# Optimization experiments

Measured on AMD Instinct MI355X. Metric: run time of the kernel, lower is better.

## Reference

```python
import jax, jax.numpy as jnp
import numpy as np

VOCAB = 200000
D = 128
B, P, R = 256, 64, 32
EPS = 1e-8


def _cos(a, b):
    # torch CosineSimilarity(dim=-1, eps=1e-8): clamp norms
    na = jnp.maximum(jnp.linalg.norm(a, axis=-1), EPS)
    nb = jnp.maximum(jnp.linalg.norm(b, axis=-1), EPS)
    return jnp.sum(a * b, axis=-1) / (na * nb)


def setup_inputs() -> dict:
    key = jax.random.key(0)
    ks = jax.random.split(key, 16)
    s = 1.0 / np.sqrt(D)
    inp = {
        "support_path": jax.random.randint(ks[0], (B, P, 3), 0, VOCAB - 1),
        "support_pair": jax.random.randint(ks[1], (B, 2), 0, VOCAB - 1),
        "support_relation_set": jax.random.randint(ks[2], (B, R), 0, VOCAB - 1),
        "emb": jax.random.normal(ks[3], (VOCAB, D), jnp.float32),
        "w_d_w": jax.random.uniform(ks[4], (D, D), jnp.float32, -s, s),
        "w_d_b": jax.random.uniform(ks[5], (D,), jnp.float32, -s, s),
        "w_e_w": jax.random.uniform(ks[6], (D, D), jnp.float32, -s, s),
        "w_e_b": jax.random.uniform(ks[7], (D,), jnp.float32, -s, s),
        "w_p_w": jax.random.uniform(ks[8], (D, D), jnp.float32, -s, s),
        "w_p_b": jax.random.uniform(ks[9], (D,), jnp.float32, -s, s),
        "e_u_w": jax.random.uniform(ks[10], (1, D), jnp.float32, -s, s),
        "e_u_b": jax.random.uniform(ks[11], (1,), jnp.float32, -s, s),
        "gru_w_ih": jax.random.uniform(ks[12], (3 * D, D), jnp.float32, -s, s),
        "gru_w_hh": jax.random.uniform(ks[13], (3 * D, D), jnp.float32, -s, s),
        "gru_b_ih": jax.random.uniform(ks[14], (3 * D,), jnp.float32, -s, s),
        "gru_b_hh": jax.random.uniform(ks[15], (3 * D,), jnp.float32, -s, s),
    }
    return inp


def _gru_cell(x, h, w_ih, w_hh, b_ih, b_hh):
    gi = x @ w_ih.T + b_ih
    gh = h @ w_hh.T + b_hh
    i_r, i_z, i_n = jnp.split(gi, 3, axis=-1)
    h_r, h_z, h_n = jnp.split(gh, 3, axis=-1)
    r = jax.nn.sigmoid(i_r + h_r)
    z = jax.nn.sigmoid(i_z + h_z)
    n = jnp.tanh(i_n + r * h_n)
    return (1.0 - z) * n + z * h


def reference(support_path, support_pair, support_relation_set, emb,
              w_d_w, w_d_b, w_e_w, w_e_b, w_p_w, w_p_b,
              e_u_w, e_u_b, gru_w_ih, gru_w_hh, gru_b_ih, gru_b_hh):
    head_emb = emb[support_pair[:, 0]]          # [B, D]
    tail_emb = emb[support_pair[:, 1]]          # [B, D]
    hts = _cos(head_emb, tail_emb)              # [B], head-tail sim per group

    rel_emb = emb[support_path]                 # [B, P, 3, D] per-step relation embeddings
    relset_emb = emb[support_relation_set]      # [B, R, D]

    # attention denominator over the group's relation set
    exp_set = jnp.exp(relset_emb @ e_u_w.T + e_u_b)        # [B, R, 1]
    sum_exp = jnp.sum(exp_set, axis=1, keepdims=True)      # [B, 1, 1]

    # entity_1/entity_2 are read from the path tensor in the original code
    e1 = rel_emb[:, :, 0, :]                                # [B, P, D]
    e2 = rel_emb[:, :, 1, :]
    h_b = head_emb[:, None, :]                              # [B, 1, D]
    t_b = tail_emb[:, None, :]
    sim_e1 = 0.5 * (_cos(h_b, e1) + _cos(t_b, e1))          # [B, P]
    sim_e2 = 0.5 * (_cos(h_b, e2) + _cos(t_b, e2))
    hts_b = hts[:, None]
    sim_rel = jnp.stack([
        0.5 * (hts_b + sim_e1),
        0.5 * (sim_e1 + sim_e2),
        0.5 * (hts_b + sim_e2),
    ], axis=-1)                                             # [B, P, 3]
    sim_dist = (1.0 - sim_rel) / 2.0                        # [B, P, 3]

    # attention score per path step
    e_score = jnp.exp(rel_emb @ e_u_w.T + e_u_b) / sum_exp[:, :, None, :]  # [B, P, 3, 1]

    d_in = rel_emb * sim_dist[..., None]
    e_in = rel_emb * e_score
    d_out = d_in @ w_d_w.T + w_d_b
    e_out = e_in @ w_e_w.T + w_e_b
    cost = 0.001 * jax.nn.relu(d_out + e_out)               # [B, P, 3, D]

    # GRU over 3 path steps, zero initial hidden
    rel_in = (rel_emb - cost) @ w_p_w.T + w_p_b             # [B, P, 3, D]
    x_steps = jnp.moveaxis(rel_in.reshape(B * P, 3, D), 1, 0)  # [3, B*P, D]

    def step(h, x):
        h2 = _gru_cell(x, h, gru_w_ih, gru_w_hh, gru_b_ih, gru_b_hh)
        return h2, None

    h0 = jnp.zeros((B * P, D), rel_in.dtype)
    h_final, _ = jax.lax.scan(step, h0, x_steps)
    return h_final.reshape(B, P, D)
```

## Files before the change

kernel.cpp:

```cpp
#include <hip/hip_runtime.h>
#include <cmath>

#define D_ 128
#define B_ 256
#define P_ 64
#define R_ 32
#define NROW (B_*P_*3)
#define NBP  (B_*P_)
#define GROWS 192
#define EPS_ 1e-8f

typedef unsigned short u16;
typedef unsigned int   u32;
using bf16x8 = __attribute__((ext_vector_type(8))) __bf16;
using f32x4  = __attribute__((ext_vector_type(4))) float;

__device__ __forceinline__ float sigm_f(float x){ return 1.0f/(1.0f + __expf(-x)); }
__device__ __forceinline__ float tanh_f(float x){
    float e = __expf(2.0f*x);
    return 1.0f - 2.0f/(e + 1.0f);
}

__device__ __forceinline__ u16 f2b(float f){
    u32 u = __builtin_bit_cast(u32, f);
    u += 0x7fffu + ((u >> 16) & 1u);
    return (u16)(u >> 16);
}
__device__ __forceinline__ float b2f(u16 s){
    return __builtin_bit_cast(float, ((u32)s) << 16);
}
__device__ __forceinline__ bf16x8 pack8(float a0,float a1,float a2,float a3,
                                        float a4,float a5,float a6,float a7){
    uint4 r;
    r.x = (u32)f2b(a0) | ((u32)f2b(a1) << 16);
    r.y = (u32)f2b(a2) | ((u32)f2b(a3) << 16);
    r.z = (u32)f2b(a4) | ((u32)f2b(a5) << 16);
    r.w = (u32)f2b(a6) | ((u32)f2b(a7) << 16);
    return __builtin_bit_cast(bf16x8, r);
}
__device__ __forceinline__ bf16x8 ldg8(const u16* p){
    return __builtin_bit_cast(bf16x8, *(const uint4*)p);
}
__device__ __forceinline__ bf16x8 ldA(const u16* Xs, int row, int gk){
    return __builtin_bit_cast(bf16x8,
        *(const uint4*)(&Xs[row*128 + ((gk ^ (row & 7)) << 3)]));
}
__device__ __forceinline__ int swz_slot(int row, int col){
    return row*128 + (((col >> 3) ^ (row & 7)) << 3) + (col & 7);
}

__global__ __launch_bounds__(1024) void k_wcvt(
    const float* __restrict__ wd, const float* __restrict__ we,
    const float* __restrict__ wp, const float* __restrict__ wih,
    const float* __restrict__ whh,
    u16* __restrict__ wdb, u16* __restrict__ web, u16* __restrict__ wpb,
    u16* __restrict__ wib, u16* __restrict__ whb)
{
    int i = blockIdx.x*1024 + threadIdx.x;
    int e = i*8;
    const float* src; u16* dst; int off;
    if      (e < 16384) { src = wd;  dst = wdb; off = e; }
    else if (e < 32768) { src = we;  dst = web; off = e - 16384; }
    else if (e < 49152) { src = wp;  dst = wpb; off = e - 32768; }
    else if (e < 98304) { src = wih; dst = wib; off = e - 49152; }
    else                { src = whh; dst = whb; off = e - 98304; }
    float4 a = *(const float4*)(src + off);
    float4 b = *(const float4*)(src + off + 4);
    uint4 r;
    r.x = (u32)f2b(a.x) | ((u32)f2b(a.y) << 16);
    r.y = (u32)f2b(a.z) | ((u32)f2b(a.w) << 16);
    r.z = (u32)f2b(b.x) | ((u32)f2b(b.y) << 16);
    r.w = (u32)f2b(b.z) | ((u32)f2b(b.w) << 16);
    *(uint4*)(dst + off) = r;
}

__global__ __launch_bounds__(512,2) void k_mega(
    const int* __restrict__ pair, const int* __restrict__ relset,
    const int* __restrict__ path,
    const float* __restrict__ emb, const float* __restrict__ eu,
    const float* __restrict__ eub,
    const u16* __restrict__ wdb, const float* __restrict__ bd,
    const u16* __restrict__ web, const float* __restrict__ be,
    const u16* __restrict__ wpb, const float* __restrict__ bpv_,
    const u16* __restrict__ wib, const u16* __restrict__ whb,
    const float* __restrict__ bih, const float* __restrict__ bhh,
    float* __restrict__ out)
{
    __shared__ u16   Xs[GROWS*128];
    __shared__ u16   Hs[64*128];
    __shared__ int   pS[GROWS];
    __shared__ float pdh[GROWS], pdt[GROWS], pdu[GROWS], pnn[GROWS];
    __shared__ float sdS[GROWS], seS[GROWS];
    __shared__ float s_hts, s_hi, s_ti;
    __shared__ float s_part[8];

    const int b    = blockIdx.x;
    const int tid  = threadIdx.x;
    const int wave = tid >> 6, lane = tid & 63;
    const int lrow = lane & 15, lk8 = lane >> 4;
    const int col  = wave*16 + lrow;
    const float eb = eub[0];

    if (tid < GROWS) pS[tid] = path[b*GROWS + tid];
    bf16x8 fD[4], fE[4], fP[4];
    #pragma unroll
    for (int ks = 0; ks < 4; ++ks) {
        const int gk = ks*4 + lk8;
        fD[ks] = ldg8(wdb + col*128 + gk*8);
        fE[ks] = ldg8(web + col*128 + gk*8);
        fP[ks] = ldg8(wpb + col*128 + gk*8);
    }
    const int ph = pair[2*b], ptl = pair[2*b+1];
    __syncthreads();

    {
        #pragma unroll
        for (int i = 0; i < 6; ++i) {
            int gid = i*512 + tid;
            int r = gid >> 4, g = gid & 15;
            const float* sp = emb + (size_t)pS[r]*128 + g*8;
            float4 f0 = *(const float4*)sp;
            float4 f1 = *(const float4*)(sp + 4);
            bf16x8 v = pack8(f0.x,f0.y,f0.z,f0.w, f1.x,f1.y,f1.z,f1.w);
            *(uint4*)(&Xs[r*128 + ((g ^ (r & 7)) << 3)]) = __builtin_bit_cast(uint4, v);
        }
        if (wave == 0) {
            float2 hv2 = *(const float2*)(emb + (size_t)ph*128 + 2*lane);
            float2 tv2 = *(const float2*)(emb + (size_t)ptl*128 + 2*lane);
            float dht = hv2.x*tv2.x + hv2.y*tv2.y;
            float dhh = hv2.x*hv2.x + hv2.y*hv2.y;
            float dtt = tv2.x*tv2.x + tv2.y*tv2.y;
            #pragma unroll
            for (int o = 32; o > 0; o >>= 1) {
                dht += __shfl_xor(dht, o);
                dhh += __shfl_xor(dhh, o);
                dtt += __shfl_xor(dtt, o);
            }
            if (lane == 0) {
                float hn = 1.f / fmaxf(sqrtf(dhh), EPS_);
                float tn = 1.f / fmaxf(sqrtf(dtt), EPS_);
                s_hts = dht*hn*tn;
                s_hi  = hn;
                s_ti  = tn;
            }
        }
        float2 uv2 = *(const float2*)(eu + 2*lane);
        float accs = 0.f;
        #pragma unroll
        for (int k = 0; k < 4; ++k) {
            const int ri = relset[b*R_ + wave*4 + k];
            float2 ev = *(const float2*)(emb + (size_t)ri*128 + 2*lane);
            float du = ev.x*uv2.x + ev.y*uv2.y;
            #pragma unroll
            for (int o = 32; o > 0; o >>= 1) du += __shfl_xor(du, o);
            accs += __expf(du + eb);
        }
        if (lane == 0) s_part[wave] = accs;
    }
    __syncthreads();

    {
        const int sub = lane >> 4, l16 = lane & 15;
        const float* hpq = emb + (size_t)ph*128  + l16*8;
        const float* tpq = emb + (size_t)ptl*128 + l16*8;
        const float* upq = eu + l16*8;
        float hq[8], tq[8], uq[8];
        {
            float4 a0 = *(const float4*)hpq, a1 = *(const float4*)(hpq+4);
            float4 b0 = *(const float4*)tpq, b1 = *(const float4*)(tpq+4);
            float4 c0 = *(const float4*)upq, c1 = *(const float4*)(upq+4);
            hq[0]=a0.x;hq[1]=a0.y;hq[2]=a0.z;hq[3]=a0.w;hq[4]=a1.x;hq[5]=a1.y;hq[6]=a1.z;hq[7]=a1.w;
            tq[0]=b0.x;tq[1]=b0.y;tq[2]=b0.z;tq[3]=b0.w;tq[4]=b1.x;tq[5]=b1.y;tq[6]=b1.z;tq[7]=b1.w;
            uq[0]=c0.x;uq[1]=c0.y;uq[2]=c0.z;uq[3]=c0.w;uq[4]=c1.x;uq[5]=c1.y;uq[6]=c1.z;uq[7]=c1.w;
        }
        #pragma unroll
        for (int i = 0; i < 6; ++i) {
            const int r = wave*24 + i*4 + sub;
            uint4 gv = *(const uint4*)(&Xs[r*128 + ((l16 ^ (r & 7)) << 3)]);
            float v[8];
            v[0]=b2f((u16)(gv.x&0xffff)); v[1]=b2f((u16)(gv.x>>16));
            v[2]=b2f((u16)(gv.y&0xffff)); v[3]=b2f((u16)(gv.y>>16));
            v[4]=b2f((u16)(gv.z&0xffff)); v[5]=b2f((u16)(gv.z>>16));
            v[6]=b2f((u16)(gv.w&0xffff)); v[7]=b2f((u16)(gv.w>>16));
            float dh=0.f, dt=0.f, du=0.f, nn=0.f;
            #pragma unroll
            for (int j = 0; j < 8; ++j) {
                dh = fmaf(v[j], hq[j], dh);
                dt = fmaf(v[j], tq[j], dt);
                du = fmaf(v[j], uq[j], du);
                nn = fmaf(v[j], v[j], nn);
            }
            #pragma unroll
            for (int o = 8; o > 0; o >>= 1) {
                dh += __shfl_xor(dh, o);
                dt += __shfl_xor(dt, o);
                du += __shfl_xor(du, o);
                nn += __shfl_xor(nn, o);
            }
            if (l16 == 0) { pdh[r]=dh; pdt[r]=dt; pdu[r]=du; pnn[r]=nn; }
        }
    }
    __syncthreads();

    if (tid < 64) {
        float is = 0.f;
        #pragma unroll
        for (int w = 0; w < 8; ++w) is += s_part[w];
        is = 1.f/is;
        const float hi = s_hi, ti = s_ti, ht = s_hts;
        const int r1 = 3*tid, r2 = r1+1, r3 = r1+2;
        float n1i = 1.f / fmaxf(sqrtf(pnn[r1]), EPS_);
        float n2i = 1.f / fmaxf(sqrtf(pnn[r2]), EPS_);
        float se1 = 0.5f*(pdh[r1]*hi + pdt[r1]*ti)*n1i;
        float se2 = 0.5f*(pdh[r2]*hi + pdt[r2]*ti)*n2i;
        sdS[r1] = (1.f - 0.5f*(ht  + se1))*0.5f;
        sdS[r2] = (1.f - 0.5f*(se1 + se2))*0.5f;
        sdS[r3] = (1.f - 0.5f*(ht  + se2))*0.5f;
        seS[r1] = expf(pdu[r1] + eb)*is;
        seS[r2] = expf(pdu[r2] + eb)*is;
        seS[r3] = expf(pdu[r3] + eb)*is;
    }
    __syncthreads();

    {
        f32x4 aD[12], aE[12];
        #pragma unroll
        for (int m = 0; m < 12; ++m) { aD[m] = (f32x4){0,0,0,0}; aE[m] = (f32x4){0,0,0,0}; }
        #pragma unroll
        for (int ks = 0; ks < 4; ++ks) {
            const int gk = ks*4 + lk8;
            #pragma unroll
            for (int mt = 0; mt < 12; ++mt) {
                bf16x8 a = ldA(Xs, mt*16 + lrow, gk);
                aD[mt] = __builtin_amdgcn_mfma_f32_16x16x32_bf16(a, fD[ks], aD[mt], 0,0,0);
                aE[mt] = __builtin_amdgcn_mfma_f32_16x16x32_bf16(a, fE[ks], aE[mt], 0,0,0);
            }
        }
        __syncthreads();
        const float bde = bd[col] + be[col];
        #pragma unroll
        for (int mt = 0; mt < 12; ++mt) {
            #pragma unroll
            for (int rr = 0; rr < 4; ++rr) {
                const int row = mt*16 + lk8*4 + rr;
                const int sl  = swz_slot(row, col);
                float relv = b2f(Xs[sl]);
                float c = sdS[row]*aD[mt][rr] + seS[row]*aE[mt][rr] + bde;
                Xs[sl] = f2b(relv - 1e-3f*fmaxf(c, 0.f));
            }
        }
    }
    __syncthreads();

    {
        f32x4 aP[12];
        #pragma unroll
        for (int m = 0; m < 12; ++m) aP[m] = (f32x4){0,0,0,0};
        #pragma unroll
        for (int ks = 0; ks < 4; ++ks) {
            const int gk = ks*4 + lk8;
            #pragma unroll
            for (int mt = 0; mt < 12; ++mt) {
                bf16x8 a = ldA(Xs, mt*16 + lrow, gk);
                aP[mt] = __builtin_amdgcn_mfma_f32_16x16x32_bf16(a, fP[ks], aP[mt], 0,0,0);
            }
        }
        __syncthreads();
        const float bpv = bpv_[col];
        #pragma unroll
        for (int mt = 0; mt < 12; ++mt) {
            #pragma unroll
            for (int rr = 0; rr < 4; ++rr) {
                const int row = mt*16 + lk8*4 + rr;
                Xs[swz_slot(row, col)] = f2b(aP[mt][rr] + bpv);
            }
        }
    }
    __syncthreads();

    bf16x8 wR[4], wZ[4], wI[4], vR[4], vZ[4], vH[4];
    #pragma unroll
    for (int ks = 0; ks < 4; ++ks) {
        const int gk = ks*4 + lk8;
        wR[ks] = ldg8(wib +           col*128 + gk*8);
        wZ[ks] = ldg8(wib + 16384   + col*128 + gk*8);
        wI[ks] = ldg8(wib + 2*16384 + col*128 + gk*8);
        vR[ks] = ldg8(whb +           col*128 + gk*8);
        vZ[ks] = ldg8(whb + 16384   + col*128 + gk*8);
        vH[ks] = ldg8(whb + 2*16384 + col*128 + gk*8);
    }
    const float brv = bih[col]       + bhh[col];
    const float bzv = bih[128 + col] + bhh[128 + col];
    const float biN = bih[256 + col];
    const float bhN = bhh[256 + col];

    float hreg[4][4];
    f32x4 aR[4], aZ[4], aI[4], aH[4];

    #pragma unroll
    for (int m = 0; m < 4; ++m) { aR[m]=(f32x4){0,0,0,0}; aZ[m]=(f32x4){0,0,0,0}; aI[m]=(f32x4){0,0,0,0}; }
    #pragma unroll
    for (int ks = 0; ks < 4; ++ks) {
        const int gk = ks*4 + lk8;
        #pragma unroll
        for (int mt = 0; mt < 4; ++mt) {
            bf16x8 ax = ldA(Xs, 3*(mt*16 + lrow) + 0, gk);
            aR[mt] = __builtin_amdgcn_mfma_f32_16x16x32_bf16(ax, wR[ks], aR[mt], 0,0,0);
            aZ[mt] = __builtin_amdgcn_mfma_f32_16x16x32_bf16(ax, wZ[ks], aZ[mt], 0,0,0);
            aI[mt] = __builtin_amdgcn_mfma_f32_16x16x32_bf16(ax, wI[ks], aI[mt], 0,0,0);
        }
    }
    #pragma unroll
    for (int mt = 0; mt < 4; ++mt)
        #pragma unroll
        for (int rr = 0; rr < 4; ++rr) {
            const int row = mt*16 + lk8*4 + rr;
            float rv = sigm_f(aR[mt][rr] + brv);
            float zv = sigm_f(aZ[mt][rr] + bzv);
            float nn = tanh_f(aI[mt][rr] + biN + rv*bhN);
            float h2 = (1.f - zv)*nn;
            hreg[mt][rr] = h2;
            Hs[swz_slot(row, col)] = f2b(h2);
        }
    __syncthreads();

    #pragma unroll
    for (int m = 0; m < 4; ++m) { aR[m]=(f32x4){0,0,0,0}; aZ[m]=(f32x4){0,0,0,0}; aI[m]=(f32x4){0,0,0,0}; aH[m]=(f32x4){0,0,0,0}; }
    #pragma unroll
    for (int ks = 0; ks < 4; ++ks) {
        const int gk = ks*4 + lk8;
        #pragma unroll
        for (int mt = 0; mt < 4; ++mt) {
            bf16x8 ax = ldA(Xs, 3*(mt*16 + lrow) + 1, gk);
            bf16x8 ah = ldA(Hs, mt*16 + lrow, gk);
            aR[mt] = __builtin_amdgcn_mfma_f32_16x16x32_bf16(ax, wR[ks], aR[mt], 0,0,0);
            aZ[mt] = __builtin_amdgcn_mfma_f32_16x16x32_bf16(ax, wZ[ks], aZ[mt], 0,0,0);
            aI[mt] = __builtin_amdgcn_mfma_f32_16x16x32_bf16(ax, wI[ks], aI[mt], 0,0,0);
            aR[mt] = __builtin_amdgcn_mfma_f32_16x16x32_bf16(ah, vR[ks], aR[mt], 0,0,0);
            aZ[mt] = __builtin_amdgcn_mfma_f32_16x16x32_bf16(ah, vZ[ks], aZ[mt], 0,0,0);
            aH[mt] = __builtin_amdgcn_mfma_f32_16x16x32_bf16(ah, vH[ks], aH[mt], 0,0,0);
        }
    }
    __syncthreads();
    #pragma unroll
    for (int mt = 0; mt < 4; ++mt)
        #pragma unroll
        for (int rr = 0; rr < 4; ++rr) {
            const int row = mt*16 + lk8*4 + rr;
            float rv = sigm_f(aR[mt][rr] + brv);
            float zv = sigm_f(aZ[mt][rr] + bzv);
            float hn = aH[mt][rr] + bhN;
            float nn = tanh_f(aI[mt][rr] + biN + rv*hn);
            float h2 = (1.f - zv)*nn + zv*hreg[mt][rr];
            hreg[mt][rr] = h2;
            Hs[swz_slot(row, col)] = f2b(h2);
        }
    __syncthreads();

    #pragma unroll
    for (int m = 0; m < 4; ++m) { aR[m]=(f32x4){0,0,0,0}; aZ[m]=(f32x4){0,0,0,0}; aI[m]=(f32x4){0,0,0,0}; aH[m]=(f32x4){0,0,0,0}; }
    #pragma unroll
    for (int ks = 0; ks < 4; ++ks) {
        const int gk = ks*4 + lk8;
        #pragma unroll
        for (int mt = 0; mt < 4; ++mt) {
            bf16x8 ax = ldA(Xs, 3*(mt*16 + lrow) + 2, gk);
            bf16x8 ah = ldA(Hs, mt*16 + lrow, gk);
            aR[mt] = __builtin_amdgcn_mfma_f32_16x16x32_bf16(ax, wR[ks], aR[mt], 0,0,0);
            aZ[mt] = __builtin_amdgcn_mfma_f32_16x16x32_bf16(ax, wZ[ks], aZ[mt], 0,0,0);
            aI[mt] = __builtin_amdgcn_mfma_f32_16x16x32_bf16(ax, wI[ks], aI[mt], 0,0,0);
            aR[mt] = __builtin_amdgcn_mfma_f32_16x16x32_bf16(ah, vR[ks], aR[mt], 0,0,0);
            aZ[mt] = __builtin_amdgcn_mfma_f32_16x16x32_bf16(ah, vZ[ks], aZ[mt], 0,0,0);
            aH[mt] = __builtin_amdgcn_mfma_f32_16x16x32_bf16(ah, vH[ks], aH[mt], 0,0,0);
        }
    }
    const int bp0 = b*64;
    #pragma unroll
    for (int mt = 0; mt < 4; ++mt)
        #pragma unroll
        for (int rr = 0; rr < 4; ++rr) {
            const int row = mt*16 + lk8*4 + rr;
            float rv = sigm_f(aR[mt][rr] + brv);
            float zv = sigm_f(aZ[mt][rr] + bzv);
            float hn = aH[mt][rr] + bhN;
            float nn = tanh_f(aI[mt][rr] + biN + rv*hn);
            float h2 = (1.f - zv)*nn + zv*hreg[mt][rr];
            out[(size_t)(bp0 + row)*128 + col] = h2;
        }
}

extern "C" void kernel_launch(void* const* d_in, const int* in_sizes, int n_in,
                              void* d_out, int out_size, void* d_ws, size_t ws_size,
                              hipStream_t stream)
{
    const int*   path   = (const int*)d_in[0];
    const int*   pair   = (const int*)d_in[1];
    const int*   relset = (const int*)d_in[2];
    const float* emb    = (const float*)d_in[3];
    const float* wd     = (const float*)d_in[4];
    const float* bd     = (const float*)d_in[5];
    const float* we     = (const float*)d_in[6];
    const float* be     = (const float*)d_in[7];
    const float* wp     = (const float*)d_in[8];
    const float* bp     = (const float*)d_in[9];
    const float* eu     = (const float*)d_in[10];
    const float* eub    = (const float*)d_in[11];
    const float* wih    = (const float*)d_in[12];
    const float* whh    = (const float*)d_in[13];
    const float* bih    = (const float*)d_in[14];
    const float* bhh    = (const float*)d_in[15];
    float* out = (float*)d_out;
    float* ws  = (float*)d_ws;

    u16* wdb = (u16*)ws;
    u16* web = wdb + 16384;
    u16* wpb = web + 16384;
    u16* wib = wpb + 16384;
    u16* whb = wib + 49152;

    k_wcvt<<<18, 1024, 0, stream>>>(wd, we, wp, wih, whh, wdb, web, wpb, wib, whb);
    k_mega<<<B_, 512, 0, stream>>>(pair, relset, path, emb, eu, eub,
                                   wdb, bd, web, be, wpb, bp,
                                   wib, whb, bih, bhh, out);
}
```

Measured before the change: 48.12 us.

## Split each batch across two blocks and fuse weight conversion into main kernel

Each batch element is now handled by two blocks of 32 paths each, doubling the grid to 512 blocks and halving shared memory and accumulator registers per block so occupancy can rise to four blocks per CU. The separate fp32-to-bf16 weight conversion kernel is removed; weights are loaded as fp32 and packed to bf16 inside the main kernel right before each GEMM, which drops one launch. Hidden-weight fragments are reloaded per GRU step to cut register pressure. In exchange every block redoes the weight conversion and the per-batch head/tail/relation-set reductions, adding redundant global loads and ALU work.

```diff
diff --git a/kernel.cpp b/kernel.cpp
--- a/kernel.cpp
+++ b/kernel.cpp
@@ -5,9 +5,7 @@
 #define B_ 256
 #define P_ 64
 #define R_ 32
-#define NROW (B_*P_*3)
-#define NBP  (B_*P_)
-#define GROWS 192
+#define HROWS 96
 #define EPS_ 1e-8f
 
 typedef unsigned short u16;
@@ -38,8 +36,10 @@
     r.w = (u32)f2b(a6) | ((u32)f2b(a7) << 16);
     return __builtin_bit_cast(bf16x8, r);
 }
-__device__ __forceinline__ bf16x8 ldg8(const u16* p){
-    return __builtin_bit_cast(bf16x8, *(const uint4*)p);
+__device__ __forceinline__ bf16x8 ldw8(const float* p){
+    float4 a = *(const float4*)p;
+    float4 b = *(const float4*)(p + 4);
+    return pack8(a.x,a.y,a.z,a.w, b.x,b.y,b.z,b.w);
 }
 __device__ __forceinline__ bf16x8 ldA(const u16* Xs, int row, int gk){
     return __builtin_bit_cast(bf16x8,
@@ -49,73 +49,42 @@
     return row*128 + (((col >> 3) ^ (row & 7)) << 3) + (col & 7);
 }
 
-__global__ __launch_bounds__(1024) void k_wcvt(
-    const float* __restrict__ wd, const float* __restrict__ we,
-    const float* __restrict__ wp, const float* __restrict__ wih,
-    const float* __restrict__ whh,
-    u16* __restrict__ wdb, u16* __restrict__ web, u16* __restrict__ wpb,
-    u16* __restrict__ wib, u16* __restrict__ whb)
-{
-    int i = blockIdx.x*1024 + threadIdx.x;
-    int e = i*8;
-    const float* src; u16* dst; int off;
-    if      (e < 16384) { src = wd;  dst = wdb; off = e; }
-    else if (e < 32768) { src = we;  dst = web; off = e - 16384; }
-    else if (e < 49152) { src = wp;  dst = wpb; off = e - 32768; }
-    else if (e < 98304) { src = wih; dst = wib; off = e - 49152; }
-    else                { src = whh; dst = whb; off = e - 98304; }
-    float4 a = *(const float4*)(src + off);
-    float4 b = *(const float4*)(src + off + 4);
-    uint4 r;
-    r.x = (u32)f2b(a.x) | ((u32)f2b(a.y) << 16);
-    r.y = (u32)f2b(a.z) | ((u32)f2b(a.w) << 16);
-    r.z = (u32)f2b(b.x) | ((u32)f2b(b.y) << 16);
-    r.w = (u32)f2b(b.z) | ((u32)f2b(b.w) << 16);
-    *(uint4*)(dst + off) = r;
-}
-
-__global__ __launch_bounds__(512,2) void k_mega(
+__global__ __launch_bounds__(512,4) void k_mega(
     const int* __restrict__ pair, const int* __restrict__ relset,
     const int* __restrict__ path,
     const float* __restrict__ emb, const float* __restrict__ eu,
     const float* __restrict__ eub,
-    const u16* __restrict__ wdb, const float* __restrict__ bd,
-    const u16* __restrict__ web, const float* __restrict__ be,
-    const u16* __restrict__ wpb, const float* __restrict__ bpv_,
-    const u16* __restrict__ wib, const u16* __restrict__ whb,
+    const float* __restrict__ wd, const float* __restrict__ bd,
+    const float* __restrict__ we, const float* __restrict__ be,
+    const float* __restrict__ wp, const float* __restrict__ bpv_,
+    const float* __restrict__ wih, const float* __restrict__ whh,
     const float* __restrict__ bih, const float* __restrict__ bhh,
     float* __restrict__ out)
 {
-    __shared__ u16   Xs[GROWS*128];
-    __shared__ u16   Hs[64*128];
-    __shared__ int   pS[GROWS];
-    __shared__ float pdh[GROWS], pdt[GROWS], pdu[GROWS], pnn[GROWS];
-    __shared__ float sdS[GROWS], seS[GROWS];
+    __shared__ u16   Xs[HROWS*128];
+    __shared__ u16   Hs[32*128];
+    __shared__ int   pS[HROWS];
+    __shared__ float pdh[HROWS], pdt[HROWS], pdu[HROWS], pnn[HROWS];
+    __shared__ float sdS[HROWS], seS[HROWS];
     __shared__ float s_hts, s_hi, s_ti;
     __shared__ float s_part[8];
 
-    const int b    = blockIdx.x;
+    const int blk  = blockIdx.x;
+    const int b    = blk >> 1;
+    const int hb   = blk & 1;
     const int tid  = threadIdx.x;
     const int wave = tid >> 6, lane = tid & 63;
     const int lrow = lane & 15, lk8 = lane >> 4;
     const int col  = wave*16 + lrow;
     const float eb = eub[0];
 
-    if (tid < GROWS) pS[tid] = path[b*GROWS + tid];
-    bf16x8 fD[4], fE[4], fP[4];
-    #pragma unroll
-    for (int ks = 0; ks < 4; ++ks) {
-        const int gk = ks*4 + lk8;
-        fD[ks] = ldg8(wdb + col*128 + gk*8);
-        fE[ks] = ldg8(web + col*128 + gk*8);
-        fP[ks] = ldg8(wpb + col*128 + gk*8);
-    }
+    if (tid < HROWS) pS[tid] = path[b*192 + hb*HROWS + tid];
     const int ph = pair[2*b], ptl = pair[2*b+1];
     __syncthreads();
 
     {
         #pragma unroll
-        for (int i = 0; i < 6; ++i) {
+        for (int i = 0; i < 3; ++i) {
             int gid = i*512 + tid;
             int r = gid >> 4, g = gid & 15;
             const float* sp = emb + (size_t)pS[r]*128 + g*8;
@@ -160,7 +129,8 @@
     __syncthreads();
 
     {
-        const int sub = lane >> 4, l16 = lane & 15;
+        const int grp = tid >> 4;
+        const int l16 = tid & 15;
         const float* hpq = emb + (size_t)ph*128  + l16*8;
         const float* tpq = emb + (size_t)ptl*128 + l16*8;
         const float* upq = eu + l16*8;
@@ -174,8 +144,8 @@
             uq[0]=c0.x;uq[1]=c0.y;uq[2]=c0.z;uq[3]=c0.w;uq[4]=c1.x;uq[5]=c1.y;uq[6]=c1.z;uq[7]=c1.w;
         }
         #pragma unroll
-        for (int i = 0; i < 6; ++i) {
-            const int r = wave*24 + i*4 + sub;
+        for (int i = 0; i < 3; ++i) {
+            const int r = i*32 + grp;
             uint4 gv = *(const uint4*)(&Xs[r*128 + ((l16 ^ (r & 7)) << 3)]);
             float v[8];
             v[0]=b2f((u16)(gv.x&0xffff)); v[1]=b2f((u16)(gv.x>>16));
@@ -202,7 +172,7 @@
     }
     __syncthreads();
 
-    if (tid < 64) {
+    if (tid < 32) {
         float is = 0.f;
         #pragma unroll
         for (int w = 0; w < 8; ++w) is += s_part[w];
@@ -223,14 +193,21 @@
     __syncthreads();
 
     {
-        f32x4 aD[12], aE[12];
-        #pragma unroll
-        for (int m = 0; m < 12; ++m) { aD[m] = (f32x4){0,0,0,0}; aE[m] = (f32x4){0,0,0,0}; }
-        #pragma unroll
-        for (int ks = 0; ks < 4; ++ks) {
-            const int gk = ks*4 + lk8;
-            #pragma unroll
-            for (int mt = 0; mt < 12; ++mt) {
+        bf16x8 fD[4], fE[4];
+        #pragma unroll
+        for (int ks = 0; ks < 4; ++ks) {
+            const int gk = ks*4 + lk8;
+            fD[ks] = ldw8(wd + col*128 + gk*8);
+            fE[ks] = ldw8(we + col*128 + gk*8);
+        }
+        f32x4 aD[6], aE[6];
+        #pragma unroll
+        for (int m = 0; m < 6; ++m) { aD[m] = (f32x4){0,0,0,0}; aE[m] = (f32x4){0,0,0,0}; }
+        #pragma unroll
+        for (int ks = 0; ks < 4; ++ks) {
+            const int gk = ks*4 + lk8;
+            #pragma unroll
+            for (int mt = 0; mt < 6; ++mt) {
                 bf16x8 a = ldA(Xs, mt*16 + lrow, gk);
                 aD[mt] = __builtin_amdgcn_mfma_f32_16x16x32_bf16(a, fD[ks], aD[mt], 0,0,0);
                 aE[mt] = __builtin_amdgcn_mfma_f32_16x16x32_bf16(a, fE[ks], aE[mt], 0,0,0);
@@ -239,7 +216,7 @@
         __syncthreads();
         const float bde = bd[col] + be[col];
         #pragma unroll
-        for (int mt = 0; mt < 12; ++mt) {
+        for (int mt = 0; mt < 6; ++mt) {
             #pragma unroll
             for (int rr = 0; rr < 4; ++rr) {
                 const int row = mt*16 + lk8*4 + rr;
@@ -253,14 +230,20 @@
     __syncthreads();
 
     {
-        f32x4 aP[12];
-        #pragma unroll
-        for (int m = 0; m < 12; ++m) aP[m] = (f32x4){0,0,0,0};
-        #pragma unroll
-        for (int ks = 0; ks < 4; ++ks) {
-            const int gk = ks*4 + lk8;
-            #pragma unroll
-            for (int mt = 0; mt < 12; ++mt) {
+        bf16x8 fP[4];
+        #pragma unroll
+        for (int ks = 0; ks < 4; ++ks) {
+            const int gk = ks*4 + lk8;
+            fP[ks] = ldw8(wp + col*128 + gk*8);
+        }
+        f32x4 aP[6];
+        #pragma unroll
+        for (int m = 0; m < 6; ++m) aP[m] = (f32x4){0,0,0,0};
+        #pragma unroll
+        for (int ks = 0; ks < 4; ++ks) {
+            const int gk = ks*4 + lk8;
+            #pragma unroll
+            for (int mt = 0; mt < 6; ++mt) {
                 bf16x8 a = ldA(Xs, mt*16 + lrow, gk);
                 aP[mt] = __builtin_amdgcn_mfma_f32_16x16x32_bf16(a, fP[ks], aP[mt], 0,0,0);
             }
@@ -268,7 +251,7 @@
         __syncthreads();
         const float bpv = bpv_[col];
         #pragma unroll
-        for (int mt = 0; mt < 12; ++mt) {
+        for (int mt = 0; mt < 6; ++mt) {
             #pragma unroll
             for (int rr = 0; rr < 4; ++rr) {
                 const int row = mt*16 + lk8*4 + rr;
@@ -278,32 +261,29 @@
     }
     __syncthreads();
 
-    bf16x8 wR[4], wZ[4], wI[4], vR[4], vZ[4], vH[4];
+    bf16x8 wR[4], wZ[4], wI[4];
     #pragma unroll
     for (int ks = 0; ks < 4; ++ks) {
         const int gk = ks*4 + lk8;
-        wR[ks] = ldg8(wib +           col*128 + gk*8);
-        wZ[ks] = ldg8(wib + 16384   + col*128 + gk*8);
-        wI[ks] = ldg8(wib + 2*16384 + col*128 + gk*8);
-        vR[ks] = ldg8(whb +           col*128 + gk*8);
-        vZ[ks] = ldg8(whb + 16384   + col*128 + gk*8);
-        vH[ks] = ldg8(whb + 2*16384 + col*128 + gk*8);
+        wR[ks] = ldw8(wih + (size_t)(      col)*128 + gk*8);
+        wZ[ks] = ldw8(wih + (size_t)(128 + col)*128 + gk*8);
+        wI[ks] = ldw8(wih + (size_t)(256 + col)*128 + gk*8);
     }
     const float brv = bih[col]       + bhh[col];
     const float bzv = bih[128 + col] + bhh[128 + col];
     const float biN = bih[256 + col];
     const float bhN = bhh[256 + col];
 
-    float hreg[4][4];
-    f32x4 aR[4], aZ[4], aI[4], aH[4];
-
-    #pragma unroll
-    for (int m = 0; m < 4; ++m) { aR[m]=(f32x4){0,0,0,0}; aZ[m]=(f32x4){0,0,0,0}; aI[m]=(f32x4){0,0,0,0}; }
+    float hreg[2][4];
+    f32x4 aR[2], aZ[2], aI[2], aH[2];
+
+    #pragma unroll
+    for (int m = 0; m < 2; ++m) { aR[m]=(f32x4){0,0,0,0}; aZ[m]=(f32x4){0,0,0,0}; aI[m]=(f32x4){0,0,0,0}; }
     #pragma unroll
     for (int ks = 0; ks < 4; ++ks) {
         const int gk = ks*4 + lk8;
         #pragma unroll
-        for (int mt = 0; mt < 4; ++mt) {
+        for (int mt = 0; mt < 2; ++mt) {
             bf16x8 ax = ldA(Xs, 3*(mt*16 + lrow) + 0, gk);
             aR[mt] = __builtin_amdgcn_mfma_f32_16x16x32_bf16(ax, wR[ks], aR[mt], 0,0,0);
             aZ[mt] = __builtin_amdgcn_mfma_f32_16x16x32_bf16(ax, wZ[ks], aZ[mt], 0,0,0);
@@ -311,7 +291,7 @@
         }
     }
     #pragma unroll
-    for (int mt = 0; mt < 4; ++mt)
+    for (int mt = 0; mt < 2; ++mt)
         #pragma unroll
         for (int rr = 0; rr < 4; ++rr) {
             const int row = mt*16 + lk8*4 + rr;
@@ -325,68 +305,59 @@
     __syncthreads();
 
     #pragma unroll
-    for (int m = 0; m < 4; ++m) { aR[m]=(f32x4){0,0,0,0}; aZ[m]=(f32x4){0,0,0,0}; aI[m]=(f32x4){0,0,0,0}; aH[m]=(f32x4){0,0,0,0}; }
-    #pragma unroll
-    for (int ks = 0; ks < 4; ++ks) {
-        const int gk = ks*4 + lk8;
-        #pragma unroll
-        for (int mt = 0; mt < 4; ++mt) {
-            bf16x8 ax = ldA(Xs, 3*(mt*16 + lrow) + 1, gk);
-            bf16x8 ah = ldA(Hs, mt*16 + lrow, gk);
-            aR[mt] = __builtin_amdgcn_mfma_f32_16x16x32_bf16(ax, wR[ks], aR[mt], 0,0,0);
-            aZ[mt] = __builtin_amdgcn_mfma_f32_16x16x32_bf16(ax, wZ[ks], aZ[mt], 0,0,0);
-            aI[mt] = __builtin_amdgcn_mfma_f32_16x16x32_bf16(ax, wI[ks], aI[mt], 0,0,0);
-            aR[mt] = __builtin_amdgcn_mfma_f32_16x16x32_bf16(ah, vR[ks], aR[mt], 0,0,0);
-            aZ[mt] = __builtin_amdgcn_mfma_f32_16x16x32_bf16(ah, vZ[ks], aZ[mt], 0,0,0);
-            aH[mt] = __builtin_amdgcn_mfma_f32_16x16x32_bf16(ah, vH[ks], aH[mt], 0,0,0);
-        }
-    }
-    __syncthreads();
-    #pragma unroll
-    for (int mt = 0; mt < 4; ++mt)
-        #pragma unroll
-        for (int rr = 0; rr < 4; ++rr) {
-            const int row = mt*16 + lk8*4 + rr;
-            float rv = sigm_f(aR[mt][rr] + brv);
-            float zv = sigm_f(aZ[mt][rr] + bzv);
-            float hn = aH[mt][rr] + bhN;
-            float nn = tanh_f(aI[mt][rr] + biN + rv*hn);
-            float h2 = (1.f - zv)*nn + zv*hreg[mt][rr];
-            hreg[mt][rr] = h2;
-            Hs[swz_slot(row, col)] = f2b(h2);
-        }
-    __syncthreads();
-
-    #pragma unroll
-    for (int m = 0; m < 4; ++m) { aR[m]=(f32x4){0,0,0,0}; aZ[m]=(f32x4){0,0,0,0}; aI[m]=(f32x4){0,0,0,0}; aH[m]=(f32x4){0,0,0,0}; }
-    #pragma unroll
-    for (int ks = 0; ks < 4; ++ks) {
-        const int gk = ks*4 + lk8;
-        #pragma unroll
-        for (int mt = 0; mt < 4; ++mt) {
-            bf16x8 ax = ldA(Xs, 3*(mt*16 + lrow) + 2, gk);
-            bf16x8 ah = ldA(Hs, mt*16 + lrow, gk);
-            aR[mt] = __builtin_amdgcn_mfma_f32_16x16x32_bf16(ax, wR[ks], aR[mt], 0,0,0);
-            aZ[mt] = __builtin_amdgcn_mfma_f32_16x16x32_bf16(ax, wZ[ks], aZ[mt], 0,0,0);
-            aI[mt] = __builtin_amdgcn_mfma_f32_16x16x32_bf16(ax, wI[ks], aI[mt], 0,0,0);
-            aR[mt] = __builtin_amdgcn_mfma_f32_16x16x32_bf16(ah, vR[ks], aR[mt], 0,0,0);
-            aZ[mt] = __builtin_amdgcn_mfma_f32_16x16x32_bf16(ah, vZ[ks], aZ[mt], 0,0,0);
-            aH[mt] = __builtin_amdgcn_mfma_f32_16x16x32_bf16(ah, vH[ks], aH[mt], 0,0,0);
-        }
-    }
-    const int bp0 = b*64;
-    #pragma unroll
-    for (int mt = 0; mt < 4; ++mt)
-        #pragma unroll
-        for (int rr = 0; rr < 4; ++rr) {
-            const int row = mt*16 + lk8*4 + rr;
-            float rv = sigm_f(aR[mt][rr] + brv);
-            float zv = sigm_f(aZ[mt][rr] + bzv);
-            float hn = aH[mt][rr] + bhN;
-            float nn = tanh_f(aI[mt][rr] + biN + rv*hn);
-            float h2 = (1.f - zv)*nn + zv*hreg[mt][rr];
-            out[(size_t)(bp0 + row)*128 + col] = h2;
-        }
+    for (int t = 1; t < 3; ++t) {
+        #pragma unroll
+        for (int m = 0; m < 2; ++m) { aR[m]=(f32x4){0,0,0,0}; aZ[m]=(f32x4){0,0,0,0}; aI[m]=(f32x4){0,0,0,0}; aH[m]=(f32x4){0,0,0,0}; }
+        #pragma unroll
+        for (int ks = 0; ks < 4; ++ks) {
+            const int gk = ks*4 + lk8;
+            bf16x8 vRk = ldw8(whh + (size_t)(      col)*128 + gk*8);
+            bf16x8 vZk = ldw8(whh + (size_t)(128 + col)*128 + gk*8);
+            bf16x8 vHk = ldw8(whh + (size_t)(256 + col)*128 + gk*8);
+            #pragma unroll
+            for (int mt = 0; mt < 2; ++mt) {
+                bf16x8 ax = ldA(Xs, 3*(mt*16 + lrow) + t, gk);
+                bf16x8 ah = ldA(Hs, mt*16 + lrow, gk);
+                aR[mt] = __builtin_amdgcn_mfma_f32_16x16x32_bf16(ax, wR[ks], aR[mt], 0,0,0);
+                aZ[mt] = __builtin_amdgcn_mfma_f32_16x16x32_bf16(ax, wZ[ks], aZ[mt], 0,0,0);
+                aI[mt] = __builtin_amdgcn_mfma_f32_16x16x32_bf16(ax, wI[ks], aI[mt], 0,0,0);
+                aR[mt] = __builtin_amdgcn_mfma_f32_16x16x32_bf16(ah, vRk, aR[mt], 0,0,0);
+                aZ[mt] = __builtin_amdgcn_mfma_f32_16x16x32_bf16(ah, vZk, aZ[mt], 0,0,0);
+                aH[mt] = __builtin_amdgcn_mfma_f32_16x16x32_bf16(ah, vHk, aH[mt], 0,0,0);
+            }
+        }
+        __syncthreads();
+        if (t < 2) {
+            #pragma unroll
+            for (int mt = 0; mt < 2; ++mt)
+                #pragma unroll
+                for (int rr = 0; rr < 4; ++rr) {
+                    const int row = mt*16 + lk8*4 + rr;
+                    float rv = sigm_f(aR[mt][rr] + brv);
+                    float zv = sigm_f(aZ[mt][rr] + bzv);
+                    float hn = aH[mt][rr] + bhN;
+                    float nn = tanh_f(aI[mt][rr] + biN + rv*hn);
+                    float h2 = (1.f - zv)*nn + zv*hreg[mt][rr];
+                    hreg[mt][rr] = h2;
+                    Hs[swz_slot(row, col)] = f2b(h2);
+                }
+            __syncthreads();
+        } else {
+            const int bp0 = b*64 + hb*32;
+            #pragma unroll
+            for (int mt = 0; mt < 2; ++mt)
+                #pragma unroll
+                for (int rr = 0; rr < 4; ++rr) {
+                    const int row = mt*16 + lk8*4 + rr;
+                    float rv = sigm_f(aR[mt][rr] + brv);
+                    float zv = sigm_f(aZ[mt][rr] + bzv);
+                    float hn = aH[mt][rr] + bhN;
+                    float nn = tanh_f(aI[mt][rr] + biN + rv*hn);
+                    float h2 = (1.f - zv)*nn + zv*hreg[mt][rr];
+                    out[(size_t)(bp0 + row)*128 + col] = h2;
+                }
+        }
+    }
 }
 
 extern "C" void kernel_launch(void* const* d_in, const int* in_sizes, int n_in,
@@ -410,16 +381,8 @@
     const float* bih    = (const float*)d_in[14];
     const float* bhh    = (const float*)d_in[15];
     float* out = (float*)d_out;
-    float* ws  = (float*)d_ws;
-
-    u16* wdb = (u16*)ws;
-    u16* web = wdb + 16384;
-    u16* wpb = web + 16384;
-    u16* wib = wpb + 16384;
-    u16* whb = wib + 49152;
-
-    k_wcvt<<<18, 1024, 0, stream>>>(wd, we, wp, wih, whh, wdb, web, wpb, wib, whb);
-    k_mega<<<B_, 512, 0, stream>>>(pair, relset, path, emb, eu, eub,
-                                   wdb, bd, web, be, wpb, bp,
-                                   wib, whb, bih, bhh, out);
-}
+
+    k_mega<<<2*B_, 512, 0, stream>>>(pair, relset, path, emb, eu, eub,
+                                     wd, bd, we, be, wp, bp,
+                                     wih, whh, bih, bhh, out);
+}
```

Result: slower. 80.85 us (+68.0%).

## Cut register pressure via per-tile GEMM loops, double LDS buffer, streamed GRU weights

Applied to the files above, without the earlier changes.

Restructures the D/E and P projection stages to process one 16-row tile at a time with small accumulators, writing the D/E result into a second LDS buffer (X2) so no barrier is needed between the MMA loads and the write-back. Weight fragments for the P projection and the GRU hidden-state weights are now loaded just before use rather than held in registers for the whole kernel, and the two GRU recurrence steps are folded into a loop. The intent is to lower VGPR pressure and avoid spills at 512 threads × 2 blocks, and to remove some barriers. In exchange, LDS use grows by 48KB per block, which may cut the number of resident blocks per CU, and the hidden-state weights are re-read from global/L2 on each step.

```diff
diff --git a/kernel.cpp b/kernel.cpp
--- a/kernel.cpp
+++ b/kernel.cpp
@@ -5,8 +5,6 @@
 #define B_ 256
 #define P_ 64
 #define R_ 32
-#define NROW (B_*P_*3)
-#define NBP  (B_*P_)
 #define GROWS 192
 #define EPS_ 1e-8f
 
@@ -87,6 +85,7 @@
     float* __restrict__ out)
 {
     __shared__ u16   Xs[GROWS*128];
+    __shared__ u16   X2[GROWS*128];
     __shared__ u16   Hs[64*128];
     __shared__ int   pS[GROWS];
     __shared__ float pdh[GROWS], pdt[GROWS], pdu[GROWS], pnn[GROWS];
@@ -102,13 +101,12 @@
     const float eb = eub[0];
 
     if (tid < GROWS) pS[tid] = path[b*GROWS + tid];
-    bf16x8 fD[4], fE[4], fP[4];
+    bf16x8 fD[4], fE[4];
     #pragma unroll
     for (int ks = 0; ks < 4; ++ks) {
         const int gk = ks*4 + lk8;
         fD[ks] = ldg8(wdb + col*128 + gk*8);
         fE[ks] = ldg8(web + col*128 + gk*8);
-        fP[ks] = ldg8(wpb + col*128 + gk*8);
     }
     const int ph = pair[2*b], ptl = pair[2*b+1];
     __syncthreads();
@@ -223,76 +221,65 @@
     __syncthreads();
 
     {
-        f32x4 aD[12], aE[12];
-        #pragma unroll
-        for (int m = 0; m < 12; ++m) { aD[m] = (f32x4){0,0,0,0}; aE[m] = (f32x4){0,0,0,0}; }
-        #pragma unroll
-        for (int ks = 0; ks < 4; ++ks) {
-            const int gk = ks*4 + lk8;
-            #pragma unroll
-            for (int mt = 0; mt < 12; ++mt) {
+        const float bde = bd[col] + be[col];
+        #pragma unroll 2
+        for (int mt = 0; mt < 12; ++mt) {
+            f32x4 aD = (f32x4){0,0,0,0}, aE = (f32x4){0,0,0,0};
+            #pragma unroll
+            for (int ks = 0; ks < 4; ++ks) {
+                const int gk = ks*4 + lk8;
                 bf16x8 a = ldA(Xs, mt*16 + lrow, gk);
-                aD[mt] = __builtin_amdgcn_mfma_f32_16x16x32_bf16(a, fD[ks], aD[mt], 0,0,0);
-                aE[mt] = __builtin_amdgcn_mfma_f32_16x16x32_bf16(a, fE[ks], aE[mt], 0,0,0);
-            }
-        }
-        __syncthreads();
-        const float bde = bd[col] + be[col];
-        #pragma unroll
-        for (int mt = 0; mt < 12; ++mt) {
+                aD = __builtin_amdgcn_mfma_f32_16x16x32_bf16(a, fD[ks], aD, 0,0,0);
+                aE = __builtin_amdgcn_mfma_f32_16x16x32_bf16(a, fE[ks], aE, 0,0,0);
+            }
             #pragma unroll
             for (int rr = 0; rr < 4; ++rr) {
                 const int row = mt*16 + lk8*4 + rr;
                 const int sl  = swz_slot(row, col);
                 float relv = b2f(Xs[sl]);
-                float c = sdS[row]*aD[mt][rr] + seS[row]*aE[mt][rr] + bde;
-                Xs[sl] = f2b(relv - 1e-3f*fmaxf(c, 0.f));
+                float c = sdS[row]*aD[rr] + seS[row]*aE[rr] + bde;
+                X2[sl] = f2b(relv - 1e-3f*fmaxf(c, 0.f));
             }
         }
     }
     __syncthreads();
 
     {
-        f32x4 aP[12];
-        #pragma unroll
-        for (int m = 0; m < 12; ++m) aP[m] = (f32x4){0,0,0,0};
-        #pragma unroll
-        for (int ks = 0; ks < 4; ++ks) {
-            const int gk = ks*4 + lk8;
-            #pragma unroll
-            for (int mt = 0; mt < 12; ++mt) {
-                bf16x8 a = ldA(Xs, mt*16 + lrow, gk);
-                aP[mt] = __builtin_amdgcn_mfma_f32_16x16x32_bf16(a, fP[ks], aP[mt], 0,0,0);
-            }
-        }
-        __syncthreads();
+        bf16x8 fP[4];
+        #pragma unroll
+        for (int ks = 0; ks < 4; ++ks)
+            fP[ks] = ldg8(wpb + col*128 + (ks*4 + lk8)*8);
         const float bpv = bpv_[col];
-        #pragma unroll
+        #pragma unroll 2
         for (int mt = 0; mt < 12; ++mt) {
+            f32x4 aP = (f32x4){0,0,0,0};
+            #pragma unroll
+            for (int ks = 0; ks < 4; ++ks) {
+                const int gk = ks*4 + lk8;
+                bf16x8 a = ldA(X2, mt*16 + lrow, gk);
+                aP = __builtin_amdgcn_mfma_f32_16x16x32_bf16(a, fP[ks], aP, 0,0,0);
+            }
             #pragma unroll
             for (int rr = 0; rr < 4; ++rr) {
                 const int row = mt*16 + lk8*4 + rr;
-                Xs[swz_slot(row, col)] = f2b(aP[mt][rr] + bpv);
-            }
-        }
-    }
-    __syncthreads();
-
-    bf16x8 wR[4], wZ[4], wI[4], vR[4], vZ[4], vH[4];
+                Xs[swz_slot(row, col)] = f2b(aP[rr] + bpv);
+            }
+        }
+    }
+
+    bf16x8 wR[4], wZ[4], wI[4];
     #pragma unroll
     for (int ks = 0; ks < 4; ++ks) {
         const int gk = ks*4 + lk8;
         wR[ks] = ldg8(wib +           col*128 + gk*8);
         wZ[ks] = ldg8(wib + 16384   + col*128 + gk*8);
         wI[ks] = ldg8(wib + 2*16384 + col*128 + gk*8);
-        vR[ks] = ldg8(whb +           col*128 + gk*8);
-        vZ[ks] = ldg8(whb + 16384   + col*128 + gk*8);
-        vH[ks] = ldg8(whb + 2*16384 + col*128 + gk*8);
     }
     const float brv = bih[col]       + bhh[col];
     const float bzv = bih[128 + col] + bhh[128 + col];
     const float biN = bih[256 + col];
     const float bhN = bhh[256 + col];
+    __syncthreads();
 
     float hreg[4][4];
     f32x4 aR[4], aZ[4], aI[4], aH[4];
@@ -325,68 +312,59 @@
     __syncthreads();
 
     #pragma unroll
-    for (int m = 0; m < 4; ++m) { aR[m]=(f32x4){0,0,0,0}; aZ[m]=(f32x4){0,0,0,0}; aI[m]=(f32x4){0,0,0,0}; aH[m]=(f32x4){0,0,0,0}; }
-    #pragma unroll
-    for (int ks = 0; ks < 4; ++ks) {
-        const int gk = ks*4 + lk8;
-        #pragma unroll
-        for (int mt = 0; mt < 4; ++mt) {
-            bf16x8 ax = ldA(Xs, 3*(mt*16 + lrow) + 1, gk);
-            bf16x8 ah = ldA(Hs, mt*16 + lrow, gk);
-            aR[mt] = __builtin_amdgcn_mfma_f32_16x16x32_bf16(ax, wR[ks], aR[mt], 0,0,0);
-            aZ[mt] = __builtin_amdgcn_mfma_f32_16x16x32_bf16(ax, wZ[ks], aZ[mt], 0,0,0);
-            aI[mt] = __builtin_amdgcn_mfma_f32_16x16x32_bf16(ax, wI[ks], aI[mt], 0,0,0);
-            aR[mt] = __builtin_amdgcn_mfma_f32_16x16x32_bf16(ah, vR[ks], aR[mt], 0,0,0);
-            aZ[mt] = __builtin_amdgcn_mfma_f32_16x16x32_bf16(ah, vZ[ks], aZ[mt], 0,0,0);
-            aH[mt] = __builtin_amdgcn_mfma_f32_16x16x32_bf16(ah, vH[ks], aH[mt], 0,0,0);
-        }
-    }
-    __syncthreads();
-    #pragma unroll
-    for (int mt = 0; mt < 4; ++mt)
-        #pragma unroll
-        for (int rr = 0; rr < 4; ++rr) {
-            const int row = mt*16 + lk8*4 + rr;
-            float rv = sigm_f(aR[mt][rr] + brv);
-            float zv = sigm_f(aZ[mt][rr] + bzv);
-            float hn = aH[mt][rr] + bhN;
-            float nn = tanh_f(aI[mt][rr] + biN + rv*hn);
-            float h2 = (1.f - zv)*nn + zv*hreg[mt][rr];
-            hreg[mt][rr] = h2;
-            Hs[swz_slot(row, col)] = f2b(h2);
-        }
-    __syncthreads();
-
-    #pragma unroll
-    for (int m = 0; m < 4; ++m) { aR[m]=(f32x4){0,0,0,0}; aZ[m]=(f32x4){0,0,0,0}; aI[m]=(f32x4){0,0,0,0}; aH[m]=(f32x4){0,0,0,0}; }
-    #pragma unroll
-    for (int ks = 0; ks < 4; ++ks) {
-        const int gk = ks*4 + lk8;
-        #pragma unroll
-        for (int mt = 0; mt < 4; ++mt) {
-            bf16x8 ax = ldA(Xs, 3*(mt*16 + lrow) + 2, gk);
-            bf16x8 ah = ldA(Hs, mt*16 + lrow, gk);
-            aR[mt] = __builtin_amdgcn_mfma_f32_16x16x32_bf16(ax, wR[ks], aR[mt], 0,0,0);
-            aZ[mt] = __builtin_amdgcn_mfma_f32_16x16x32_bf16(ax, wZ[ks], aZ[mt], 0,0,0);
-            aI[mt] = __builtin_amdgcn_mfma_f32_16x16x32_bf16(ax, wI[ks], aI[mt], 0,0,0);
-            aR[mt] = __builtin_amdgcn_mfma_f32_16x16x32_bf16(ah, vR[ks], aR[mt], 0,0,0);
-            aZ[mt] = __builtin_amdgcn_mfma_f32_16x16x32_bf16(ah, vZ[ks], aZ[mt], 0,0,0);
-            aH[mt] = __builtin_amdgcn_mfma_f32_16x16x32_bf16(ah, vH[ks], aH[mt], 0,0,0);
-        }
-    }
-    const int bp0 = b*64;
-    #pragma unroll
-    for (int mt = 0; mt < 4; ++mt)
-        #pragma unroll
-        for (int rr = 0; rr < 4; ++rr) {
-            const int row = mt*16 + lk8*4 + rr;
-            float rv = sigm_f(aR[mt][rr] + brv);
-            float zv = sigm_f(aZ[mt][rr] + bzv);
-            float hn = aH[mt][rr] + bhN;
-            float nn = tanh_f(aI[mt][rr] + biN + rv*hn);
-            float h2 = (1.f - zv)*nn + zv*hreg[mt][rr];
-            out[(size_t)(bp0 + row)*128 + col] = h2;
-        }
+    for (int t = 1; t < 3; ++t) {
+        #pragma unroll
+        for (int m = 0; m < 4; ++m) { aR[m]=(f32x4){0,0,0,0}; aZ[m]=(f32x4){0,0,0,0}; aI[m]=(f32x4){0,0,0,0}; aH[m]=(f32x4){0,0,0,0}; }
+        #pragma unroll
+        for (int ks = 0; ks < 4; ++ks) {
+            const int gk = ks*4 + lk8;
+            bf16x8 vRk = ldg8(whb +           col*128 + gk*8);
+            bf16x8 vZk = ldg8(whb + 16384   + col*128 + gk*8);
+            bf16x8 vHk = ldg8(whb + 2*16384 + col*128 + gk*8);
+            #pragma unroll
+            for (int mt = 0; mt < 4; ++mt) {
+                bf16x8 ax = ldA(Xs, 3*(mt*16 + lrow) + t, gk);
+                bf16x8 ah = ldA(Hs, mt*16 + lrow, gk);
+                aR[mt] = __builtin_amdgcn_mfma_f32_16x16x32_bf16(ax, wR[ks], aR[mt], 0,0,0);
+                aZ[mt] = __builtin_amdgcn_mfma_f32_16x16x32_bf16(ax, wZ[ks], aZ[mt], 0,0,0);
+                aI[mt] = __builtin_amdgcn_mfma_f32_16x16x32_bf16(ax, wI[ks], aI[mt], 0,0,0);
+                aR[mt] = __builtin_amdgcn_mfma_f32_16x16x32_bf16(ah, vRk, aR[mt], 0,0,0);
+                aZ[mt] = __builtin_amdgcn_mfma_f32_16x16x32_bf16(ah, vZk, aZ[mt], 0,0,0);
+                aH[mt] = __builtin_amdgcn_mfma_f32_16x16x32_bf16(ah, vHk, aH[mt], 0,0,0);
+            }
+        }
+        __syncthreads();
+        if (t < 2) {
+            #pragma unroll
+            for (int mt = 0; mt < 4; ++mt)
+                #pragma unroll
+                for (int rr = 0; rr < 4; ++rr) {
+                    const int row = mt*16 + lk8*4 + rr;
+                    float rv = sigm_f(aR[mt][rr] + brv);
+                    float zv = sigm_f(aZ[mt][rr] + bzv);
+                    float hn = aH[mt][rr] + bhN;
+                    float nn = tanh_f(aI[mt][rr] + biN + rv*hn);
+                    float h2 = (1.f - zv)*nn + zv*hreg[mt][rr];
+                    hreg[mt][rr] = h2;
+                    Hs[swz_slot(row, col)] = f2b(h2);
+                }
+            __syncthreads();
+        } else {
+            const int bp0 = b*64;
+            #pragma unroll
+            for (int mt = 0; mt < 4; ++mt)
+                #pragma unroll
+                for (int rr = 0; rr < 4; ++rr) {
+                    const int row = mt*16 + lk8*4 + rr;
+                    float rv = sigm_f(aR[mt][rr] + brv);
+                    float zv = sigm_f(aZ[mt][rr] + bzv);
+                    float hn = aH[mt][rr] + bhN;
+                    float nn = tanh_f(aI[mt][rr] + biN + rv*hn);
+                    float h2 = (1.f - zv)*nn + zv*hreg[mt][rr];
+                    out[(size_t)(bp0 + row)*128 + col] = h2;
+                }
+        }
+    }
 }
 
 extern "C" void kernel_launch(void* const* d_in, const int* in_sizes, int n_in,
```

After: 44.23 us. -8.1%, faster.
